# Performance work log

Hardware: AMD Instinct MI355X
Metric: run time of the kernel (lower is better)

## Reference

```python
import jax, jax.numpy as jnp
import numpy as np

B, T, F_IN = 4, 2048, 768
G, V = 2, 320          # num_groups, num_vars per group
VQ_DIM = 256
D = VQ_DIM // G        # var_dim = 128


def setup_inputs() -> dict:
    key = jax.random.key(0)
    k1, k2, k3 = jax.random.split(key, 3)
    x = jax.random.normal(k1, (B, T, F_IN), dtype=jnp.float32)
    # weight_proj: Linear(input_dim -> G*V), weight init N(0,1), bias zeros
    W = jax.random.normal(k2, (G * V, F_IN), dtype=jnp.float32)
    b = jnp.zeros((G * V,), dtype=jnp.float32)
    # self.vars: uniform_(0,1), stored here reshaped as [G, V, D]
    codebook = jax.random.uniform(k3, (G, V, D), dtype=jnp.float32)
    return {"x": x, "W": W, "b": b, "codebook": codebook}


def reference(x, W, b, codebook):
    bsz, tsz, fsz = x.shape
    g, v, d = codebook.shape
    # projection to logits over (group, codeword)
    logits = (x.reshape(-1, fsz) @ W.T + b).reshape(-1, g, v)  # [BT, G, V]
    k = jnp.argmax(logits, axis=-1)                            # [BT, G] int
    # hard one-hot stats (code perplexity)
    hard = jax.nn.one_hot(k, v, dtype=jnp.float32)             # [BT, G, V]
    hard_probs = hard.mean(axis=0)                             # [G, V]
    code_perplexity = jnp.exp(-jnp.sum(hard_probs * jnp.log(hard_probs + 1e-7), axis=-1)).sum()
    # soft stats (prob perplexity)
    avg_probs = jax.nn.softmax(logits.astype(jnp.float32), axis=-1).mean(axis=0)  # [G, V]
    prob_perplexity = jnp.exp(-jnp.sum(avg_probs * jnp.log(avg_probs + 1e-7), axis=-1)).sum()
    # eval path: hard one-hot times codebook summed == direct gather of codewords
    xq = codebook[jnp.arange(g)[None, :], k]                   # [BT, G, D]
    xq = xq.reshape(bsz, tsz, g * d)                           # [B, T, vq_dim]
    return xq, g * v, code_perplexity, prob_perplexity
```

## Files before the change

### kernel.cpp

```cpp
#include <hip/hip_runtime.h>
#include <hip/hip_bf16.h>

#define NROWS 8192
#define KDIM  768
#define VSZ   320
#define GSZ   2
#define NCOL  640
#define DSZ   128
#define BM    64
#define NMT   (NROWS / BM)
#define NBLK  (NMT * 2)
#define NKB   24
#define XQ_TOTAL (NROWS * GSZ * DSZ)
#define MARGIN 0.75f
#define XBLKS 3072
#define WBLKS 240

typedef __attribute__((ext_vector_type(8))) short bf16x8;
typedef __attribute__((ext_vector_type(4))) float f32x4;

static __device__ __forceinline__ short f2bf(float f) {
    union { __hip_bfloat16 h; short s; } u;
    u.h = __float2bfloat16(f);
    return u.s;
}

static __device__ __forceinline__ void gload_lds16(const void* g, void* l) {
    __builtin_amdgcn_global_load_lds(
        (const __attribute__((address_space(1))) void*)g,
        (__attribute__((address_space(3))) void*)l, 16, 0, 0);
}

__global__ __launch_bounds__(256) void prep_k(const float* __restrict__ x,
                                              const float* __restrict__ W,
                                              short* __restrict__ Xb,
                                              short* __restrict__ Wb,
                                              float* __restrict__ accf) {
    const int bid = blockIdx.x;
    if (bid == 0) {
        for (int i = threadIdx.x; i < 2 * NCOL; i += 256) accf[i] = 0.f;
    }
    const float* src;
    short* dst;
    int id, row, k;
    if (bid < XBLKS) {
        id = bid * 256 + threadIdx.x;
        const int lane = id & 63;
        const int f    = id >> 6;
        const int rblk = f / NKB;
        const int kb   = f - rblk * NKB;
        row = rblk * 16 + (lane & 15);
        k   = kb * 32 + (lane >> 4) * 8;
        src = x; dst = Xb;
    } else {
        id = (bid - XBLKS) * 256 + threadIdx.x;
        const int lane = id & 63;
        const int f    = id >> 6;
        const int n    = f % 5;
        const int t2   = f / 5;
        const int hc   = t2 & 7;
        const int kb   = t2 >> 3;
        row = (hc * 5 + n) * 16 + (lane & 15);
        k   = kb * 32 + (lane >> 4) * 8;
        src = W; dst = Wb;
    }
    const float4 a = *(const float4*)(src + (size_t)row * KDIM + k);
    const float4 c = *(const float4*)(src + (size_t)row * KDIM + k + 4);
    bf16x8 r;
    r[0] = f2bf(a.x); r[1] = f2bf(a.y); r[2] = f2bf(a.z); r[3] = f2bf(a.w);
    r[4] = f2bf(c.x); r[5] = f2bf(c.y); r[6] = f2bf(c.z); r[7] = f2bf(c.w);
    *(bf16x8*)(dst + (size_t)id * 8) = r;
}

#define STAGE(kb32, BUF) do {                                                  \
    _Pragma("unroll")                                                          \
    for (int j = 0; j < 3; ++j) {                                              \
        const int f = w + 8 * j;                                               \
        const short* src;                                                      \
        if (f < 4) {                                                           \
            src = Xb + ((size_t)(mt * 4 + f) * 24 + (kb32)) * 512;             \
        } else {                                                               \
            const int rm = f - 4;                                              \
            src = Wb + ((size_t)((kb32) * 8 + hc0 + rm / 5) * 5 + rm % 5) * 512; \
        }                                                                      \
        gload_lds16(src + lane * 8, (char*)(BUF) + f * 1024);                  \
    }                                                                          \
} while (0)

#define COMPUTE(BUF) do {                                                      \
    const char* _bp = (const char*)(BUF);                                      \
    const bf16x8 a0 = *(const bf16x8*)(_bp + (rs * 2 + 0) * 1024 + lane * 16); \
    const bf16x8 a1 = *(const bf16x8*)(_bp + (rs * 2 + 1) * 1024 + lane * 16); \
    bf16x8 bb[5];                                                              \
    _Pragma("unroll")                                                          \
    for (int n = 0; n < 5; ++n)                                                \
        bb[n] = *(const bf16x8*)(_bp + 4096 + (cc * 5 + n) * 1024 + lane * 16);\
    _Pragma("unroll")                                                          \
    for (int n = 0; n < 5; ++n) {                                              \
        acc[0][n] = __builtin_amdgcn_mfma_f32_16x16x32_bf16(a0, bb[n], acc[0][n], 0, 0, 0); \
        acc[1][n] = __builtin_amdgcn_mfma_f32_16x16x32_bf16(a1, bb[n], acc[1][n], 0, 0, 0); \
    }                                                                          \
} while (0)

#define SYNCN do {                                                             \
    asm volatile("s_waitcnt vmcnt(3)" ::: "memory");                           \
    __builtin_amdgcn_sched_barrier(0);                                         \
    __builtin_amdgcn_s_barrier();                                              \
} while (0)
#define SYNC0 do {                                                             \
    asm volatile("s_waitcnt vmcnt(0)" ::: "memory");                           \
    __builtin_amdgcn_sched_barrier(0);                                         \
    __builtin_amdgcn_s_barrier();                                              \
} while (0)

__global__ __launch_bounds__(512, 4) void fused_vq_k(
    const short* __restrict__ Xb, const short* __restrict__ Wb,
    const float* __restrict__ x, const float* __restrict__ W,
    const float* __restrict__ b, const float* __restrict__ codebook,
    float* __restrict__ accf, float* __restrict__ xq) {

    __shared__ __align__(16) char bufs[2][24 * 1024];
    __shared__ float pacc[2][VSZ];
    __shared__ float cnt_f[VSZ];
    __shared__ float wmax[BM][4];
    __shared__ int   warg[BM][4];
    __shared__ float ssum[BM][4];
    __shared__ float rmax_s[BM];
    __shared__ int   rarg_s[BM];
    __shared__ int   cnt_s[BM];
    __shared__ int   list_s[BM][16];
    __shared__ int   code_s[BM];
    __shared__ int   work_s[BM];
    __shared__ int   nwork_s;

    const int tid   = threadIdx.x;
    const int lane  = tid & 63;
    const int w     = tid >> 6;
    const int l15   = lane & 15;
    const int l4    = lane >> 4;
    const int sb    = ((int)blockIdx.x & 7) * (NBLK / 8) + ((int)blockIdx.x >> 3);
    const int mt    = sb >> 1;
    const int h     = sb & 1;
    const int row0  = mt * BM;
    const int rs    = w >> 2;
    const int cc    = w & 3;
    const int hc0   = h * 4;
    const int nf0   = h * 20 + cc * 5;

    for (int i = tid; i < VSZ; i += 512) cnt_f[i] = 0.f;
    if (tid < BM) cnt_s[tid] = 0;
    if (tid == 0) nwork_s = 0;

    char* B0 = bufs[0];
    char* B1 = bufs[1];

    f32x4 acc[2][5];
#pragma unroll
    for (int hh = 0; hh < 2; ++hh)
#pragma unroll
        for (int n = 0; n < 5; ++n) acc[hh][n] = (f32x4){0.f, 0.f, 0.f, 0.f};

    STAGE(0, B0);
    __syncthreads();

#pragma unroll 1
    for (int t = 0; t < 11; ++t) {
        STAGE(2 * t + 1, B1); COMPUTE(B0); SYNCN;
        STAGE(2 * t + 2, B0); COMPUTE(B1); SYNCN;
    }
    STAGE(23, B1); COMPUTE(B0); SYNC0;
    COMPUTE(B1);

#pragma unroll
    for (int n = 0; n < 5; ++n) {
        const float bv = b[(nf0 + n) * 16 + l15];
#pragma unroll
        for (int hh = 0; hh < 2; ++hh)
#pragma unroll
            for (int r = 0; r < 4; ++r) acc[hh][n][r] += bv;
    }

    float m4[2][4]; int a4[2][4];
#pragma unroll
    for (int hh = 0; hh < 2; ++hh)
#pragma unroll
        for (int r = 0; r < 4; ++r) { m4[hh][r] = -3.4e38f; a4[hh][r] = 0x7fffffff; }
#pragma unroll
    for (int n = 0; n < 5; ++n) {
        const int col = (nf0 + n) * 16 + l15;
#pragma unroll
        for (int hh = 0; hh < 2; ++hh)
#pragma unroll
            for (int r = 0; r < 4; ++r) {
                const float v = acc[hh][n][r];
                if (v > m4[hh][r]) { m4[hh][r] = v; a4[hh][r] = col; }
            }
    }
#pragma unroll
    for (int off = 8; off >= 1; off >>= 1)
#pragma unroll
        for (int hh = 0; hh < 2; ++hh)
#pragma unroll
            for (int r = 0; r < 4; ++r) {
                const float om = __shfl_xor(m4[hh][r], off);
                const int   oa = __shfl_xor(a4[hh][r], off);
                if (om > m4[hh][r] || (om == m4[hh][r] && oa < a4[hh][r])) {
                    m4[hh][r] = om; a4[hh][r] = oa;
                }
            }
    if (l15 == 0)
#pragma unroll
        for (int hh = 0; hh < 2; ++hh)
#pragma unroll
            for (int r = 0; r < 4; ++r) {
                const int row = rs * 32 + hh * 16 + l4 * 4 + r;
                wmax[row][cc] = m4[hh][r];
                warg[row][cc] = a4[hh][r];
            }
    __syncthreads();

    if (tid < BM) {
        float m = -3.4e38f; int c = 0x7fffffff;
#pragma unroll
        for (int q = 0; q < 4; ++q) {
            const float mq = wmax[tid][q];
            const int   cq = warg[tid][q];
            if (mq > m || (mq == m && cq < c)) { m = mq; c = cq; }
        }
        rmax_s[tid] = m;
        rarg_s[tid] = c;
    }
    __syncthreads();

    float rm[2][4];
#pragma unroll
    for (int hh = 0; hh < 2; ++hh)
#pragma unroll
        for (int r = 0; r < 4; ++r) rm[hh][r] = rmax_s[rs * 32 + hh * 16 + l4 * 4 + r];
    float sden[2][4] = {{0.f,0.f,0.f,0.f},{0.f,0.f,0.f,0.f}};
#pragma unroll
    for (int n = 0; n < 5; ++n) {
        const int col = (nf0 + n) * 16 + l15;
#pragma unroll
        for (int hh = 0; hh < 2; ++hh)
#pragma unroll
            for (int r = 0; r < 4; ++r) {
                const float v = acc[hh][n][r];
                if (v > rm[hh][r] - MARGIN) {
                    const int row = rs * 32 + hh * 16 + l4 * 4 + r;
                    const int idx = atomicAdd(&cnt_s[row], 1);
                    if (idx < 16) list_s[row][idx] = col;
                }
                const float e = __expf(v - rm[hh][r]);
                acc[hh][n][r] = e;
                sden[hh][r] += e;
            }
    }
#pragma unroll
    for (int off = 8; off >= 1; off >>= 1)
#pragma unroll
        for (int hh = 0; hh < 2; ++hh)
#pragma unroll
            for (int r = 0; r < 4; ++r) sden[hh][r] += __shfl_xor(sden[hh][r], off);
    if (l15 == 0)
#pragma unroll
        for (int hh = 0; hh < 2; ++hh)
#pragma unroll
            for (int r = 0; r < 4; ++r)
                ssum[rs * 32 + hh * 16 + l4 * 4 + r][cc] = sden[hh][r];
    __syncthreads();

    if (tid < BM) {
        if (cnt_s[tid] <= 1) {
            code_s[tid] = rarg_s[tid];
        } else {
            const int wi = atomicAdd(&nwork_s, 1);
            work_s[wi] = tid;
        }
    }

    float inv[2][4];
#pragma unroll
    for (int hh = 0; hh < 2; ++hh)
#pragma unroll
        for (int r = 0; r < 4; ++r) {
            const int row = rs * 32 + hh * 16 + l4 * 4 + r;
            inv[hh][r] = 1.f / (ssum[row][0] + ssum[row][1] + ssum[row][2] + ssum[row][3]);
        }
#pragma unroll
    for (int n = 0; n < 5; ++n) {
        float pc = 0.f;
#pragma unroll
        for (int hh = 0; hh < 2; ++hh)
#pragma unroll
            for (int r = 0; r < 4; ++r) pc += acc[hh][n][r] * inv[hh][r];
        pc += __shfl_xor(pc, 16);
        pc += __shfl_xor(pc, 32);
        if (l4 == 0) pacc[rs][(nf0 + n) * 16 + l15 - h * VSZ] = pc;
    }
    __syncthreads();

    const int nwork = nwork_s;
    for (int it = w; it < nwork; it += 8) {
        const int row  = work_s[it];
        const int grow = row0 + row;
        const int nc   = min(cnt_s[row], 16);
        const float4* xr = (const float4*)(x + (size_t)grow * KDIM);
        float bestv = -3.4e38f; int bestc = 0x7fffffff;
        for (int ci = 0; ci < nc; ++ci) {
            const int col = list_s[row][ci];
            const float4* wr = (const float4*)(W + (size_t)col * KDIM);
            float p = 0.f;
#pragma unroll
            for (int j = 0; j < 3; ++j) {
                const float4 xv = xr[lane + 64 * j];
                const float4 wv = wr[lane + 64 * j];
                p += xv.x * wv.x + xv.y * wv.y + xv.z * wv.z + xv.w * wv.w;
            }
#pragma unroll
            for (int off = 32; off >= 1; off >>= 1) p += __shfl_xor(p, off);
            p += b[col];
            if (p > bestv || (p == bestv && col < bestc)) { bestv = p; bestc = col; }
        }
        if (lane == 0) code_s[row] = bestc;
    }
    __syncthreads();

    if (tid < BM) atomicAdd(&cnt_f[code_s[tid] - h * VSZ], 1.f);

#pragma unroll
    for (int u = 0; u < 4; ++u) {
        const int f   = tid + u * 512;
        const int row = f >> 5;
        const int d4  = (f & 31) * 4;
        const int k   = code_s[row];
        const float4 v = *(const float4*)(codebook + (size_t)k * DSZ + d4);
        *(float4*)(xq + (size_t)(row0 + row) * (GSZ * DSZ) + h * DSZ + d4) = v;
    }
    __syncthreads();

    for (int i = tid; i < VSZ; i += 512) {
        atomicAdd(&accf[h * VSZ + i], cnt_f[i]);
        atomicAdd(&accf[NCOL + h * VSZ + i], pacc[0][i] + pacc[1][i]);
    }
}

__global__ __launch_bounds__(640) void finalize_k(const float* __restrict__ accf,
                                                  float* __restrict__ out_scalars) {
    __shared__ float se_c[GSZ], se_p[GSZ];
    const int t = threadIdx.x;
    if (t < GSZ) { se_c[t] = 0.f; se_p[t] = 0.f; }
    __syncthreads();
    const int g = t / VSZ;
    const float hp = accf[t]        * (1.f / (float)NROWS);
    const float ap = accf[NCOL + t] * (1.f / (float)NROWS);
    float tc = hp * logf(hp + 1e-7f);
    float tp = ap * logf(ap + 1e-7f);
#pragma unroll
    for (int off = 32; off >= 1; off >>= 1) {
        tc += __shfl_xor(tc, off);
        tp += __shfl_xor(tp, off);
    }
    if ((t & 63) == 0) { atomicAdd(&se_c[g], tc); atomicAdd(&se_p[g], tp); }
    __syncthreads();
    if (t == 0) {
        out_scalars[0] = (float)NCOL;
        out_scalars[1] = expf(-se_c[0]) + expf(-se_c[1]);
        out_scalars[2] = expf(-se_p[0]) + expf(-se_p[1]);
    }
}

extern "C" void kernel_launch(void* const* d_in, const int* in_sizes, int n_in,
                              void* d_out, int out_size, void* d_ws, size_t ws_size,
                              hipStream_t stream) {
    const float* x        = (const float*)d_in[0];
    const float* W        = (const float*)d_in[1];
    const float* b        = (const float*)d_in[2];
    const float* codebook = (const float*)d_in[3];
    float* out = (float*)d_out;

    short* Wb   = (short*)d_ws;
    short* Xb   = (short*)((char*)d_ws + 983040);
    float* accf = (float*)((char*)d_ws + 983040 + 12582912);

    prep_k<<<dim3(XBLKS + WBLKS), dim3(256), 0, stream>>>(x, W, Xb, Wb, accf);
    fused_vq_k<<<dim3(NBLK), dim3(512), 0, stream>>>(Xb, Wb, x, W, b, codebook,
                                                     accf, out);
    finalize_k<<<dim3(1), dim3(640), 0, stream>>>(accf, out + XQ_TOTAL);
}
```

Before: 46.33 us.

## Fuse x bf16 conversion into GEMM mainloop, drop separate X prep pass

The prep kernel no longer converts the whole x matrix to a bf16 MFMA-tiled buffer. Only W is still pre-converted. Inside the fused kernel each thread loads fp32 x directly, converts it to bf16 in registers and writes it into the LDS A tile, with register prefetch one k-step ahead. This removes a 25MB fp32 read plus a 12.5MB bf16 write-then-reread of x. The cost is that each of the two column-half blocks converts the same rows, so x is read twice in fp32, and the barrier now also waits on LDS writes.

```diff
diff --git a/kernel.cpp b/kernel.cpp
--- a/kernel.cpp
+++ b/kernel.cpp
@@ -13,8 +13,6 @@
 #define NKB   24
 #define XQ_TOTAL (NROWS * GSZ * DSZ)
 #define MARGIN 0.75f
-#define XBLKS 3072
-#define WBLKS 240
 
 typedef __attribute__((ext_vector_type(8))) short bf16x8;
 typedef __attribute__((ext_vector_type(4))) float f32x4;
@@ -31,60 +29,44 @@
         (__attribute__((address_space(3))) void*)l, 16, 0, 0);
 }
 
-__global__ __launch_bounds__(256) void prep_k(const float* __restrict__ x,
-                                              const float* __restrict__ W,
-                                              short* __restrict__ Xb,
-                                              short* __restrict__ Wb,
-                                              float* __restrict__ accf) {
-    const int bid = blockIdx.x;
-    if (bid == 0) {
+__global__ __launch_bounds__(256) void prep_w_k(const float* __restrict__ W,
+                                                short* __restrict__ Wb,
+                                                float* __restrict__ accf) {
+    if (blockIdx.x == 0) {
         for (int i = threadIdx.x; i < 2 * NCOL; i += 256) accf[i] = 0.f;
     }
-    const float* src;
-    short* dst;
-    int id, row, k;
-    if (bid < XBLKS) {
-        id = bid * 256 + threadIdx.x;
-        const int lane = id & 63;
-        const int f    = id >> 6;
-        const int rblk = f / NKB;
-        const int kb   = f - rblk * NKB;
-        row = rblk * 16 + (lane & 15);
-        k   = kb * 32 + (lane >> 4) * 8;
-        src = x; dst = Xb;
-    } else {
-        id = (bid - XBLKS) * 256 + threadIdx.x;
-        const int lane = id & 63;
-        const int f    = id >> 6;
-        const int n    = f % 5;
-        const int t2   = f / 5;
-        const int hc   = t2 & 7;
-        const int kb   = t2 >> 3;
-        row = (hc * 5 + n) * 16 + (lane & 15);
-        k   = kb * 32 + (lane >> 4) * 8;
-        src = W; dst = Wb;
-    }
-    const float4 a = *(const float4*)(src + (size_t)row * KDIM + k);
-    const float4 c = *(const float4*)(src + (size_t)row * KDIM + k + 4);
+    const int id   = blockIdx.x * 256 + threadIdx.x;
+    const int lane = id & 63;
+    const int f    = id >> 6;
+    const int n    = f % 5;
+    const int t2   = f / 5;
+    const int hc   = t2 & 7;
+    const int kb   = t2 >> 3;
+    const int col  = (hc * 5 + n) * 16 + (lane & 15);
+    const int k    = kb * 32 + (lane >> 4) * 8;
+    const float4 a = *(const float4*)(W + (size_t)col * KDIM + k);
+    const float4 c = *(const float4*)(W + (size_t)col * KDIM + k + 4);
     bf16x8 r;
     r[0] = f2bf(a.x); r[1] = f2bf(a.y); r[2] = f2bf(a.z); r[3] = f2bf(a.w);
     r[4] = f2bf(c.x); r[5] = f2bf(c.y); r[6] = f2bf(c.z); r[7] = f2bf(c.w);
-    *(bf16x8*)(dst + (size_t)id * 8) = r;
-}
-
-#define STAGE(kb32, BUF) do {                                                  \
+    *(bf16x8*)(Wb + (size_t)id * 8) = r;
+}
+
+#define STAGEB(kb32, BUF) do {                                                 \
     _Pragma("unroll")                                                          \
     for (int j = 0; j < 3; ++j) {                                              \
-        const int f = w + 8 * j;                                               \
-        const short* src;                                                      \
-        if (f < 4) {                                                           \
-            src = Xb + ((size_t)(mt * 4 + f) * 24 + (kb32)) * 512;             \
-        } else {                                                               \
-            const int rm = f - 4;                                              \
-            src = Wb + ((size_t)((kb32) * 8 + hc0 + rm / 5) * 5 + rm % 5) * 512; \
-        }                                                                      \
-        gload_lds16(src + lane * 8, (char*)(BUF) + f * 1024);                  \
+        const int rm = (j == 0) ? w : (j == 1) ? (w + 8) : (16 + (w & 3));     \
+        const short* srcp = Wb + ((size_t)((kb32) * 8 + hc0 + rm / 5) * 5 + rm % 5) * 512; \
+        gload_lds16(srcp + lane * 8, (char*)(BUF) + 4096 + rm * 1024);         \
     }                                                                          \
+} while (0)
+
+#define AWRITE(BUF, v) do {                                                    \
+    const short s0 = f2bf((v).x), s1 = f2bf((v).y);                            \
+    const short s2 = f2bf((v).z), s3 = f2bf((v).w);                            \
+    const int lo = (s0 & 0xffff) | ((int)s1 << 16);                            \
+    const int hi = (s2 & 0xffff) | ((int)s3 << 16);                            \
+    *(int2*)((char*)(BUF) + a_off) = make_int2(lo, hi);                        \
 } while (0)
 
 #define COMPUTE(BUF) do {                                                      \
@@ -102,19 +84,14 @@
     }                                                                          \
 } while (0)
 
-#define SYNCN do {                                                             \
-    asm volatile("s_waitcnt vmcnt(3)" ::: "memory");                           \
+#define SYNC(N) do {                                                           \
+    asm volatile("s_waitcnt vmcnt(" #N ") lgkmcnt(0)" ::: "memory");           \
     __builtin_amdgcn_sched_barrier(0);                                         \
     __builtin_amdgcn_s_barrier();                                              \
 } while (0)
-#define SYNC0 do {                                                             \
-    asm volatile("s_waitcnt vmcnt(0)" ::: "memory");                           \
-    __builtin_amdgcn_sched_barrier(0);                                         \
-    __builtin_amdgcn_s_barrier();                                              \
-} while (0)
 
 __global__ __launch_bounds__(512, 4) void fused_vq_k(
-    const short* __restrict__ Xb, const short* __restrict__ Wb,
+    const short* __restrict__ Wb,
     const float* __restrict__ x, const float* __restrict__ W,
     const float* __restrict__ b, const float* __restrict__ codebook,
     float* __restrict__ accf, float* __restrict__ xq) {
@@ -147,6 +124,11 @@
     const int hc0   = h * 4;
     const int nf0   = h * 20 + cc * 5;
 
+    const int arow  = tid >> 3;
+    const int akk   = (tid & 7) * 4;
+    const int a_off = (arow >> 4) * 1024 + ((arow & 15) + 16 * (akk >> 3)) * 16 + (akk & 4) * 2;
+    const float* xrow = x + (size_t)(row0 + arow) * KDIM + akk;
+
     for (int i = tid; i < VSZ; i += 512) cnt_f[i] = 0.f;
     if (tid < BM) cnt_s[tid] = 0;
     if (tid == 0) nwork_s = 0;
@@ -160,15 +142,26 @@
 #pragma unroll
         for (int n = 0; n < 5; ++n) acc[hh][n] = (f32x4){0.f, 0.f, 0.f, 0.f};
 
-    STAGE(0, B0);
-    __syncthreads();
+    float4 xv = *(const float4*)(xrow);
+    AWRITE(B0, xv);
+    STAGEB(0, B0);
+    xv = *(const float4*)(xrow + 32);
+    SYNC(1);
 
 #pragma unroll 1
-    for (int t = 0; t < 11; ++t) {
-        STAGE(2 * t + 1, B1); COMPUTE(B0); SYNCN;
-        STAGE(2 * t + 2, B0); COMPUTE(B1); SYNCN;
-    }
-    STAGE(23, B1); COMPUTE(B0); SYNC0;
+    for (int k = 0; k < 22; ++k) {
+        char* bufn = bufs[0] + (((k + 1) & 1) * 24576);
+        char* bufc = bufs[0] + ((k & 1) * 24576);
+        AWRITE(bufn, xv);
+        STAGEB(k + 1, bufn);
+        xv = *(const float4*)(xrow + (k + 2) * 32);
+        COMPUTE(bufc);
+        SYNC(1);
+    }
+    AWRITE(B1, xv);
+    STAGEB(23, B1);
+    COMPUTE(B0);
+    SYNC(0);
     COMPUTE(B1);
 
 #pragma unroll
@@ -313,9 +306,9 @@
             float p = 0.f;
 #pragma unroll
             for (int j = 0; j < 3; ++j) {
-                const float4 xv = xr[lane + 64 * j];
-                const float4 wv = wr[lane + 64 * j];
-                p += xv.x * wv.x + xv.y * wv.y + xv.z * wv.z + xv.w * wv.w;
+                const float4 xv2 = xr[lane + 64 * j];
+                const float4 wv2 = wr[lane + 64 * j];
+                p += xv2.x * wv2.x + xv2.y * wv2.y + xv2.z * wv2.z + xv2.w * wv2.w;
             }
 #pragma unroll
             for (int off = 32; off >= 1; off >>= 1) p += __shfl_xor(p, off);
@@ -380,11 +373,10 @@
     float* out = (float*)d_out;
 
     short* Wb   = (short*)d_ws;
-    short* Xb   = (short*)((char*)d_ws + 983040);
-    float* accf = (float*)((char*)d_ws + 983040 + 12582912);
-
-    prep_k<<<dim3(XBLKS + WBLKS), dim3(256), 0, stream>>>(x, W, Xb, Wb, accf);
-    fused_vq_k<<<dim3(NBLK), dim3(512), 0, stream>>>(Xb, Wb, x, W, b, codebook,
+    float* accf = (float*)((char*)d_ws + 983040);
+
+    prep_w_k<<<dim3(240), dim3(256), 0, stream>>>(W, Wb, accf);
+    fused_vq_k<<<dim3(NBLK), dim3(512), 0, stream>>>(Wb, x, W, b, codebook,
                                                      accf, out);
     finalize_k<<<dim3(1), dim3(640), 0, stream>>>(accf, out + XQ_TOTAL);
 }
```

Result: faster. 45.17 us (-2.5%).
